# Performance work log

Measured on AMD Instinct MI355X. Metric: run time of the kernel, lower is better.

The kernel has to match this reference:

```python
import jax, jax.numpy as jnp
import numpy as np

NUM_CLASSES = 19
PROJ_DIM = 128
QUEUE_LEN = 2975
B, H, W = 8, 128, 128
EPS = 1e-12  # torch F.normalize eps


def setup_inputs() -> dict:
    key = jax.random.key(0)
    k0, k1, k2, k3, k4 = jax.random.split(key, 5)
    proj3 = jax.random.normal(k0, (B, PROJ_DIM, H, W), jnp.float32)
    proj4 = jax.random.normal(k1, (B, PROJ_DIM, H, W), jnp.float32)
    proj5 = jax.random.normal(k2, (B, PROJ_DIM, H, W), jnp.float32)
    logits = jax.random.normal(k3, (B, NUM_CLASSES, H, W), jnp.float32)
    q = jax.random.normal(k4, (3, NUM_CLASSES, PROJ_DIM, QUEUE_LEN), jnp.float32)
    # buffers are L2-normalized along proj_dim at init
    queues = q / jnp.maximum(jnp.linalg.norm(q, axis=2, keepdims=True), EPS)
    return {"proj3": proj3, "proj4": proj4, "proj5": proj5,
            "logits": logits, "queues": queues}


def _region_keys(fea, pred):
    """fea: (D, HW) float, pred: (HW,) int. Masked mean per class, L2-normalized."""
    onehot = (pred[None, :] == jnp.arange(NUM_CLASSES)[:, None]).astype(fea.dtype)  # (C, HW)
    counts = onehot.sum(1)                                   # (C,)
    sums = jnp.einsum('ch,dh->cd', onehot, fea)              # (C, D)
    present = counts > 0
    means = sums / jnp.maximum(counts, 1.0)[:, None]
    keys = means / jnp.maximum(jnp.linalg.norm(means, axis=1, keepdims=True), EPS)
    return keys, present


def _contrast_loss(keys, present, queue):
    """keys: (C, D), queue: (C, D, L) (detached in original). Sum over present classes."""
    q = jax.lax.stop_gradient(queue)
    # (query . queue_col) implemented as elementwise-mul + mean over D in the original
    sim = jnp.einsum('cd,kdl->ckl', keys, q) / PROJ_DIM      # (C, C, L)
    ar = jnp.arange(NUM_CLASSES)
    pos = sim[ar, ar, :]                                     # (C, L)  l_pos per class
    exp_all = jnp.exp(sim)
    s_neg = exp_all.sum(axis=(1, 2)) - exp_all[ar, ar, :].sum(1)  # scalar neg mass per class
    loss_c = -(pos - jnp.log(jnp.exp(pos) + s_neg[:, None])).sum(1) / QUEUE_LEN
    return jnp.where(present, loss_c, 0.0).sum()


def _enqueue(queue, ptr, keys, present):
    """Write key into queue column ptr[c] for present classes, advance ptr by 1."""
    ar = jnp.arange(NUM_CLASSES)
    cur = queue[ar, :, ptr]                                  # (C, D)
    newcol = jnp.where(present[:, None], jax.lax.stop_gradient(keys), cur)
    queue = queue.at[ar, :, ptr].set(newcol)
    ptr = jnp.where(present, (ptr + 1) % QUEUE_LEN, ptr)
    return queue, ptr


def reference(proj3, proj4, proj5, logits, queues):
    pred = jnp.argmax(logits, axis=1).reshape(B, -1)         # (B, HW)
    total = jnp.float32(0.0)
    for pi, projector in enumerate((proj3, proj4, proj5)):
        fea_all = projector.reshape(B, PROJ_DIM, -1)          # (B, D, HW)

        def step(carry, inp):
            queue, ptr, acc = carry
            f, p = inp
            keys, present = _region_keys(f, p)
            acc = acc + _contrast_loss(keys, present, queue)
            queue, ptr = _enqueue(queue, ptr, keys, present)
            return (queue, ptr, acc), None

        init = (queues[pi], jnp.zeros((NUM_CLASSES,), jnp.int32), jnp.float32(0.0))
        (_, _, acc), _ = jax.lax.scan(step, init, (fea_all, pred))
        total = total + acc / B
    return total
```

## Files before the change

kernel.cpp:

```cpp
#include <hip/hip_runtime.h>
#include <stdint.h>

#define NCLS 19
#define PDIM 128
#define QLEN 2975
#define BATCH 8
#define HW 16384
#define ROWS 152
#define ROWS_PAD 160
#define LT2 64
#define HCHUNK 512

typedef __attribute__((ext_vector_type(8))) short short8;
typedef __attribute__((ext_vector_type(4))) float floatx4;

__device__ __forceinline__ uint16_t f2b(float f) {
    uint32_t u = __float_as_uint(f);
    uint32_t r = (u + 0x7FFFu + ((u >> 16) & 1u)) >> 16;
    return (uint16_t)r;
}

__global__ __launch_bounds__(256)
void k_pred(const float* __restrict__ logits, uint8_t* __restrict__ pred,
            int* __restrict__ counts) {
    __shared__ int cnt[NCLS];
    int tid = threadIdx.x;
    if (tid < NCLS) cnt[tid] = 0;
    __syncthreads();
    int idx = blockIdx.x * 256 + tid;
    int b = idx >> 14, h = idx & (HW - 1);
    const float* base = logits + (size_t)b * NCLS * HW + h;
    float best = base[0];
    int bi = 0;
#pragma unroll
    for (int c = 1; c < NCLS; ++c) {
        float v = base[(size_t)c * HW];
        if (v > best) { best = v; bi = c; }
    }
    pred[idx] = (uint8_t)bi;
    atomicAdd(&cnt[bi], 1);
    __syncthreads();
    if (tid < NCLS) atomicAdd(&counts[b * NCLS + tid], cnt[tid]);
}

__global__ __launch_bounds__(512)
void k_msum(const float* __restrict__ p0, const float* __restrict__ p1,
            const float* __restrict__ p2, const uint8_t* __restrict__ pred,
            float* __restrict__ sums) {
    int chunk = blockIdx.x, b = blockIdx.y, pi = blockIdx.z;
    const float* proj = (pi == 0) ? p0 : (pi == 1) ? p1 : p2;
    int tid = threadIdx.x;
    int wave = tid >> 6, lane = tid & 63;
    int col = lane & 15, g = lane >> 4;
    int d = wave * 16 + col;
    int h0 = chunk * HCHUNK;

    const float* frow = proj + ((size_t)b * PDIM + d) * HW;
    const uint8_t* pr = pred + (size_t)b * HW + h0;

    floatx4 acc0 = (floatx4)(0.f);
    floatx4 acc1 = (floatx4)(0.f);

#pragma unroll 4
    for (int s = 0; s < HCHUNK / 32; ++s) {
        int hk = h0 + s * 32 + g * 8;
        union { float4 f; uint4 u; } va, vb;
        va.f = *(const float4*)(frow + hk);
        vb.f = *(const float4*)(frow + hk + 4);
        uint64_t pb = *(const uint64_t*)(pr + s * 32 + g * 8);

        union { short8 s8; uint32_t w[4]; } bf;
        bf.w[0] = __builtin_amdgcn_perm(va.u.y, va.u.x, 0x07060302u);
        bf.w[1] = __builtin_amdgcn_perm(va.u.w, va.u.z, 0x07060302u);
        bf.w[2] = __builtin_amdgcn_perm(vb.u.y, vb.u.x, 0x07060302u);
        bf.w[3] = __builtin_amdgcn_perm(vb.u.w, vb.u.z, 0x07060302u);

        union { short8 s8; uint16_t h[8]; } a0, a1;
#pragma unroll
        for (int j = 0; j < 8; ++j) {
            int cb = (int)((pb >> (8 * j)) & 0xFF);
            a0.h[j] = (cb == col)      ? (uint16_t)0x3F80 : (uint16_t)0;
            a1.h[j] = (cb == col + 16) ? (uint16_t)0x3F80 : (uint16_t)0;
        }
        acc0 = __builtin_amdgcn_mfma_f32_16x16x32_bf16(a0.s8, bf.s8, acc0, 0, 0, 0);
        acc1 = __builtin_amdgcn_mfma_f32_16x16x32_bf16(a1.s8, bf.s8, acc1, 0, 0, 0);
    }

    float* sb = sums + (((size_t)pi * BATCH + b) * NCLS) * PDIM + d;
#pragma unroll
    for (int r = 0; r < 4; ++r) {
        int row0 = g * 4 + r;
        atomicAdd(&sb[(size_t)row0 * PDIM], acc0[r]);
        int row1 = 16 + g * 4 + r;
        if (row1 < NCLS) atomicAdd(&sb[(size_t)row1 * PDIM], acc1[r]);
    }
}

__global__ __launch_bounds__(64)
void k_keys(const float* __restrict__ sums, const int* __restrict__ counts,
            uint16_t* __restrict__ keysb) {
    int c = blockIdx.x, b = blockIdx.y, pi = blockIdx.z;
    int lane = threadIdx.x;
    size_t base = (((size_t)pi * BATCH + b) * NCLS + c) * PDIM;
    int cn = counts[b * NCLS + c];
    float cnt = (float)(cn > 0 ? cn : 1);
    float m0 = sums[base + lane] / cnt;
    float m1 = sums[base + lane + 64] / cnt;
    float nr = m0 * m0 + m1 * m1;
    for (int off = 32; off; off >>= 1) nr += __shfl_xor(nr, off);
    float scale = 1.f / fmaxf(sqrtf(nr), 1e-12f);
    size_t bb = ((size_t)pi * ROWS_PAD + b * NCLS + c) * PDIM;
    keysb[bb + lane]      = f2b(m0 * scale);
    keysb[bb + lane + 64] = f2b(m1 * scale);
}

__global__ __launch_bounds__(256)
void k_sim(const float* __restrict__ q, const uint16_t* __restrict__ keysb,
           float* __restrict__ Sall, float* __restrict__ D0,
           float* __restrict__ pos0) {
    __shared__ short keys[ROWS_PAD * 136];
    __shared__ float rowsum[ROWS_PAD];
    int tile = blockIdx.x, k = blockIdx.y, pi = blockIdx.z;
    int tid = threadIdx.x;
    int wave = tid >> 6, lane = tid & 63;
    int col = lane & 15, g = lane >> 4;

    {
        const uint32_t* kg = (const uint32_t*)(keysb + (size_t)pi * ROWS_PAD * PDIM);
        uint32_t* kl = (uint32_t*)keys;
        for (int j = tid; j < ROWS_PAD * 64; j += 256) {
            int r = j >> 6, dw = j & 63;
            kl[r * 68 + dw] = kg[j];
        }
    }
    if (tid < ROWS_PAD) rowsum[tid] = 0.f;
    __syncthreads();

    int l = tile * LT2 + wave * 16 + col;
    bool lok = l < QLEN;
    int lc = lok ? l : (QLEN - 1);
    const float* qk = q + ((size_t)pi * NCLS + k) * (size_t)PDIM * QLEN + lc;

    floatx4 acc[10];
#pragma unroll
    for (int m = 0; m < 10; ++m) acc[m] = (floatx4)(0.f);

#pragma unroll
    for (int s = 0; s < 4; ++s) {
        union { float f[8]; uint32_t u[8]; } v;
#pragma unroll
        for (int j = 0; j < 8; ++j)
            v.f[j] = qk[(size_t)(s * 32 + g * 8 + j) * QLEN];
        union { short8 s8; uint32_t w[4]; } bf;
        bf.w[0] = __builtin_amdgcn_perm(v.u[1], v.u[0], 0x07060302u);
        bf.w[1] = __builtin_amdgcn_perm(v.u[3], v.u[2], 0x07060302u);
        bf.w[2] = __builtin_amdgcn_perm(v.u[5], v.u[4], 0x07060302u);
        bf.w[3] = __builtin_amdgcn_perm(v.u[7], v.u[6], 0x07060302u);
#pragma unroll
        for (int m = 0; m < 10; ++m) {
            short8 af = *(const short8*)&keys[(m * 16 + col) * 136 + s * 32 + g * 8];
            acc[m] = __builtin_amdgcn_mfma_f32_16x16x32_bf16(af, bf.s8, acc[m], 0, 0, 0);
        }
    }

    const float inv = 1.f / (float)PDIM;
#pragma unroll
    for (int m = 0; m < 10; ++m) {
#pragma unroll
        for (int r = 0; r < 4; ++r) {
            int row = m * 16 + g * 4 + r;
            float sim = acc[m][r] * inv;
            float e = (lok && row < ROWS) ? __expf(sim) : 0.f;
#pragma unroll
            for (int off = 1; off < 16; off <<= 1) e += __shfl_xor(e, off);
            if (col == 0 && row < ROWS) atomicAdd(&rowsum[row], e);
            if (lok && row < ROWS) {
                int bb = row / NCLS, cc = row - bb * NCLS;
                if (cc == k)
                    pos0[(((size_t)pi * BATCH + bb) * NCLS + cc) * QLEN + l] = sim;
            }
        }
    }
    __syncthreads();
    if (tid < ROWS) {
        float v = rowsum[tid];
        atomicAdd(&Sall[pi * ROWS + tid], v);
        int cc = tid % NCLS;
        if (cc == k) atomicAdd(&D0[pi * ROWS + tid], v);
    }
}

__global__ __launch_bounds__(256)
void k_loss(const float* __restrict__ pos0, const float* __restrict__ Sall,
            const float* __restrict__ D0, const int* __restrict__ counts,
            float* __restrict__ out) {
    int c = blockIdx.x, b = blockIdx.y, pi = blockIdx.z;
    if (counts[b * NCLS + c] <= 0) return;
    int tid = threadIdx.x;
    int row = b * NCLS + c;
    float sneg = Sall[pi * ROWS + row] - D0[pi * ROWS + row];
    const float* pp = pos0 + (((size_t)pi * BATCH + b) * NCLS + c) * QLEN;
    float sum = 0.f;
    for (int l = tid; l < QLEN; l += 256) {
        float p = pp[l];
        sum += p - logf(__expf(p) + sneg);
    }
    __shared__ float red[4];
    int wave = tid >> 6, lane = tid & 63;
    for (int off = 32; off; off >>= 1) sum += __shfl_down(sum, off);
    if (lane == 0) red[wave] = sum;
    __syncthreads();
    if (tid == 0) {
        float t = red[0] + red[1] + red[2] + red[3];
        atomicAdd(out, -t / ((float)QLEN * (float)BATCH));
    }
}

extern "C" void kernel_launch(void* const* d_in, const int* in_sizes, int n_in,
                              void* d_out, int out_size, void* d_ws, size_t ws_size,
                              hipStream_t stream) {
    const float* proj3  = (const float*)d_in[0];
    const float* proj4  = (const float*)d_in[1];
    const float* proj5  = (const float*)d_in[2];
    const float* logits = (const float*)d_in[3];
    const float* queues = (const float*)d_in[4];

    char* ws = (char*)d_ws;
    int*      counts = (int*)ws;
    uint8_t*  pred   = (uint8_t*)(ws + 1024);
    float*    sums   = (float*)(ws + 1024 + 131072);
    uint16_t* keysb  = (uint16_t*)(ws + 365568);
    float*    Sall   = (float*)(ws + 488448);
    float*    D0f    = (float*)(ws + 490496);
    float*    pos0   = (float*)(ws + 492544);

    hipMemsetAsync(ws, 0, 492544, stream);
    hipMemsetAsync(d_out, 0, sizeof(float), stream);

    k_pred<<<dim3(512), 256, 0, stream>>>(logits, pred, counts);

    dim3 gs(32, BATCH, 3);
    k_msum<<<gs, 512, 0, stream>>>(proj3, proj4, proj5, pred, sums);

    dim3 gk(NCLS, BATCH, 3);
    k_keys<<<gk, 64, 0, stream>>>(sums, counts, keysb);

    dim3 gm((QLEN + LT2 - 1) / LT2, NCLS, 3);
    k_sim<<<gm, 256, 0, stream>>>(queues, keysb, Sall, D0f, pos0);

    dim3 gl(NCLS, BATCH, 3);
    k_loss<<<gl, 256, 0, stream>>>(pos0, Sall, D0f, counts, (float*)d_out);
}
```

Measured before the change: 157.8 us.

## Double queue columns per k_sim block and swizzle keys LDS layout

```diff
diff --git a/kernel.cpp b/kernel.cpp
--- a/kernel.cpp
+++ b/kernel.cpp
@@ -8,7 +8,6 @@
 #define HW 16384
 #define ROWS 152
 #define ROWS_PAD 160
-#define LT2 64
 #define HCHUNK 512
 
 typedef __attribute__((ext_vector_type(8))) short short8;
@@ -114,54 +113,75 @@
     keysb[bb + lane + 64] = f2b(m1 * scale);
 }
 
-__global__ __launch_bounds__(256)
+__global__ __launch_bounds__(256, 4)
 void k_sim(const float* __restrict__ q, const uint16_t* __restrict__ keysb,
            float* __restrict__ Sall, float* __restrict__ D0,
            float* __restrict__ pos0) {
-    __shared__ short keys[ROWS_PAD * 136];
-    __shared__ float rowsum[ROWS_PAD];
+    __shared__ char smem[40960];
     int tile = blockIdx.x, k = blockIdx.y, pi = blockIdx.z;
     int tid = threadIdx.x;
     int wave = tid >> 6, lane = tid & 63;
     int col = lane & 15, g = lane >> 4;
 
     {
-        const uint32_t* kg = (const uint32_t*)(keysb + (size_t)pi * ROWS_PAD * PDIM);
-        uint32_t* kl = (uint32_t*)keys;
-        for (int j = tid; j < ROWS_PAD * 64; j += 256) {
-            int r = j >> 6, dw = j & 63;
-            kl[r * 68 + dw] = kg[j];
-        }
-    }
+        const uint4* kg = (const uint4*)(keysb + (size_t)pi * ROWS_PAD * PDIM);
+        uint4* kl = (uint4*)smem;
+        int kgrp = tid & 15;
+        int r0 = tid >> 4;
+#pragma unroll
+        for (int it = 0; it < 10; ++it) {
+            int row = r0 + it * 16;
+            kl[kgrp * 160 + (row ^ (kgrp & 7))] = kg[row * 16 + kgrp];
+        }
+    }
+    __syncthreads();
+
+    int l0 = tile * 128 + wave * 16 + col;
+    int l1 = l0 + 64;
+    bool okA = l0 < QLEN, okB = l1 < QLEN;
+    const float* qbase = q + ((size_t)pi * NCLS + k) * (size_t)PDIM * QLEN;
+    const float* qA = qbase + (okA ? l0 : (QLEN - 1));
+    const float* qB = qbase + (okB ? l1 : (QLEN - 1));
+
+    floatx4 accA[10], accB[10];
+#pragma unroll
+    for (int m = 0; m < 10; ++m) { accA[m] = (floatx4)(0.f); accB[m] = (floatx4)(0.f); }
+
+    const short8* kls = (const short8*)smem;
+#pragma unroll
+    for (int s = 0; s < 4; ++s) {
+        union { float f[8]; uint32_t u[8]; } va, vb;
+#pragma unroll
+        for (int j = 0; j < 8; ++j) {
+            size_t off = (size_t)(s * 32 + g * 8 + j) * QLEN;
+            va.f[j] = qA[off];
+            vb.f[j] = qB[off];
+        }
+        union { short8 s8; uint32_t w[4]; } bfA, bfB;
+        bfA.w[0] = __builtin_amdgcn_perm(va.u[1], va.u[0], 0x07060302u);
+        bfA.w[1] = __builtin_amdgcn_perm(va.u[3], va.u[2], 0x07060302u);
+        bfA.w[2] = __builtin_amdgcn_perm(va.u[5], va.u[4], 0x07060302u);
+        bfA.w[3] = __builtin_amdgcn_perm(va.u[7], va.u[6], 0x07060302u);
+        bfB.w[0] = __builtin_amdgcn_perm(vb.u[1], vb.u[0], 0x07060302u);
+        bfB.w[1] = __builtin_amdgcn_perm(vb.u[3], vb.u[2], 0x07060302u);
+        bfB.w[2] = __builtin_amdgcn_perm(vb.u[5], vb.u[4], 0x07060302u);
+        bfB.w[3] = __builtin_amdgcn_perm(vb.u[7], vb.u[6], 0x07060302u);
+
+        int kgrp = s * 4 + g;
+        int kxor = kgrp & 7;
+        const short8* kp = kls + (size_t)kgrp * 160;
+#pragma unroll
+        for (int m = 0; m < 10; ++m) {
+            short8 af = kp[(m * 16 + col) ^ kxor];
+            accA[m] = __builtin_amdgcn_mfma_f32_16x16x32_bf16(af, bfA.s8, accA[m], 0, 0, 0);
+            accB[m] = __builtin_amdgcn_mfma_f32_16x16x32_bf16(af, bfB.s8, accB[m], 0, 0, 0);
+        }
+    }
+
+    __syncthreads();
+    float* rowsum = (float*)smem;
     if (tid < ROWS_PAD) rowsum[tid] = 0.f;
     __syncthreads();
-
-    int l = tile * LT2 + wave * 16 + col;
-    bool lok = l < QLEN;
-    int lc = lok ? l : (QLEN - 1);
-    const float* qk = q + ((size_t)pi * NCLS + k) * (size_t)PDIM * QLEN + lc;
-
-    floatx4 acc[10];
-#pragma unroll
-    for (int m = 0; m < 10; ++m) acc[m] = (floatx4)(0.f);
-
-#pragma unroll
-    for (int s = 0; s < 4; ++s) {
-        union { float f[8]; uint32_t u[8]; } v;
-#pragma unroll
-        for (int j = 0; j < 8; ++j)
-            v.f[j] = qk[(size_t)(s * 32 + g * 8 + j) * QLEN];
-        union { short8 s8; uint32_t w[4]; } bf;
-        bf.w[0] = __builtin_amdgcn_perm(v.u[1], v.u[0], 0x07060302u);
-        bf.w[1] = __builtin_amdgcn_perm(v.u[3], v.u[2], 0x07060302u);
-        bf.w[2] = __builtin_amdgcn_perm(v.u[5], v.u[4], 0x07060302u);
-        bf.w[3] = __builtin_amdgcn_perm(v.u[7], v.u[6], 0x07060302u);
-#pragma unroll
-        for (int m = 0; m < 10; ++m) {
-            short8 af = *(const short8*)&keys[(m * 16 + col) * 136 + s * 32 + g * 8];
-            acc[m] = __builtin_amdgcn_mfma_f32_16x16x32_bf16(af, bf.s8, acc[m], 0, 0, 0);
-        }
-    }
 
     const float inv = 1.f / (float)PDIM;
 #pragma unroll
@@ -169,15 +189,21 @@
 #pragma unroll
         for (int r = 0; r < 4; ++r) {
             int row = m * 16 + g * 4 + r;
-            float sim = acc[m][r] * inv;
-            float e = (lok && row < ROWS) ? __expf(sim) : 0.f;
+            bool rok = row < ROWS;
+            float sA = accA[m][r] * inv;
+            float sB = accB[m][r] * inv;
+            float e = 0.f;
+            if (rok) e = (okA ? __expf(sA) : 0.f) + (okB ? __expf(sB) : 0.f);
 #pragma unroll
             for (int off = 1; off < 16; off <<= 1) e += __shfl_xor(e, off);
-            if (col == 0 && row < ROWS) atomicAdd(&rowsum[row], e);
-            if (lok && row < ROWS) {
+            if (col == 0 && rok) atomicAdd(&rowsum[row], e);
+            if (rok) {
                 int bb = row / NCLS, cc = row - bb * NCLS;
-                if (cc == k)
-                    pos0[(((size_t)pi * BATCH + bb) * NCLS + cc) * QLEN + l] = sim;
+                if (cc == k) {
+                    float* pb = pos0 + (((size_t)pi * BATCH + bb) * NCLS + cc) * QLEN;
+                    if (okA) pb[l0] = sA;
+                    if (okB) pb[l1] = sB;
+                }
             }
         }
     }
@@ -245,7 +271,7 @@
     dim3 gk(NCLS, BATCH, 3);
     k_keys<<<gk, 64, 0, stream>>>(sums, counts, keysb);
 
-    dim3 gm((QLEN + LT2 - 1) / LT2, NCLS, 3);
+    dim3 gm((QLEN + 127) / 128, NCLS, 3);
     k_sim<<<gm, 256, 0, stream>>>(queues, keysb, Sall, D0f, pos0);
 
     dim3 gl(NCLS, BATCH, 3);
```

Result: faster. 150.9 us (-4.4%).
